# Performance work log

Hardware: AMD Instinct MI355X
Metric: run time of the kernel (lower is better)

The kernel has to match this reference:

```python
import jax, jax.numpy as jnp
import numpy as np
from jax import lax


def setup_inputs() -> dict:
    key = jax.random.key(0)
    ks = jax.random.split(key, 12)
    B, T_dec, T_enc, E, H, V = 32, 64, 128, 256, 512, 32000
    s = 0.05
    emb_W = jax.random.normal(ks[0], (V, E), jnp.float32) * s
    emb_W = emb_W.at[0].set(0.0)  # padding_idx=0
    return {
        "dec_X": jax.random.randint(ks[1], (B, T_dec), 0, V, dtype=jnp.int64),
        "enc_output": jax.random.normal(ks[2], (B, T_enc, H), jnp.float32),
        "h0": jax.random.normal(ks[3], (1, B, H), jnp.float32),
        "c0": jax.random.normal(ks[4], (1, B, H), jnp.float32),
        "emb_W": emb_W,
        "W_ih": jax.random.normal(ks[5], (4 * H, E), jnp.float32) * s,
        "W_hh": jax.random.normal(ks[6], (4 * H, H), jnp.float32) * s,
        "b_ih": jax.random.normal(ks[7], (4 * H,), jnp.float32) * s,
        "b_hh": jax.random.normal(ks[8], (4 * H,), jnp.float32) * s,
        "attn_W": jax.random.normal(ks[9], (H, 2 * H), jnp.float32) * s,
        "attn_b": jax.random.normal(ks[10], (H,), jnp.float32) * s,
        "fc_W": jax.random.normal(ks[11], (V, H), jnp.float32) * s,
        "fc_b": jnp.zeros((V,), jnp.float32),
    }


def reference(dec_X, enc_output, h0, c0, emb_W, W_ih, W_hh, b_ih, b_hh,
              attn_W, attn_b, fc_W, fc_b):
    # Embedding lookup for all decoder steps at once; padding_idx=0 -> zero vector.
    emb = emb_W[dec_X] * (dec_X != 0)[..., None].astype(emb_W.dtype)  # [B, T_dec, E]
    h, c = h0[0], c0[0]  # [B, H] (num_layers == 1)
    bias = b_ih + b_hh

    def step(carry, x_t):  # x_t: [B, E]
        h, c = carry
        g = x_t @ W_ih.T + h @ W_hh.T + bias          # [B, 4H]
        i, f, gg, o = jnp.split(g, 4, axis=-1)        # torch gate order i,f,g,o
        c = jax.nn.sigmoid(f) * c + jax.nn.sigmoid(i) * jnp.tanh(gg)
        h = jax.nn.sigmoid(o) * jnp.tanh(c)           # dec_rnn_out
        # dot-product attention over encoder timesteps (softmax over dim 1)
        scores = jnp.einsum('bth,bh->bt', enc_output, h)   # [B, T_enc]
        a = jax.nn.softmax(scores, axis=1)
        c_t = jnp.einsum('bt,bth->bh', a, enc_output)       # [B, H]
        cat = jnp.concatenate([h, c_t], axis=-1)            # [B, 2H]
        out = jnp.tanh(cat @ attn_W.T + attn_b)             # [B, H]
        logits = out @ fc_W.T + fc_b                        # [B, V]
        return (h, c), logits

    (h, c), logits = lax.scan(step, (h, c), jnp.swapaxes(emb, 0, 1))
    output = jnp.swapaxes(logits, 0, 1)  # [B, T_dec, V]
    return output, (h[None], c[None])
```

## Files before the change

kernel.cpp:

```cpp
#include <hip/hip_runtime.h>
#include <cstdint>
#include <cstddef>

typedef unsigned short u16;
typedef short s8v __attribute__((ext_vector_type(8)));
typedef float f4v __attribute__((ext_vector_type(4)));

static __device__ __forceinline__ u16 f2bf(float x) {
  union { float f; uint32_t u; } v; v.f = x;
  uint32_t r = v.u + 0x7fffu + ((v.u >> 16) & 1u);
  return (u16)(r >> 16);
}
static __device__ __forceinline__ uint2 f2bf4(float4 v) {
  uint2 r;
  r.x = (uint32_t)f2bf(v.x) | ((uint32_t)f2bf(v.y) << 16);
  r.y = (uint32_t)f2bf(v.z) | ((uint32_t)f2bf(v.w) << 16);
  return r;
}
static __device__ __forceinline__ float sigm(float x) { return 1.0f / (1.0f + __expf(-x)); }

typedef __attribute__((address_space(3))) uint32_t lds_u32;
typedef const __attribute__((address_space(1))) uint32_t glb_u32;
static __device__ __forceinline__ void gload16(const void* g, void* l) {
  __builtin_amdgcn_global_load_lds((glb_u32*)g, (lds_u32*)l, 16, 0, 0);
}

__global__ void kPrep(const float* __restrict__ fcW, const float* __restrict__ attnW,
                      const float* __restrict__ Wih, const float* __restrict__ bih,
                      const float* __restrict__ bhh, const float* __restrict__ embW,
                      const int* __restrict__ decX,
                      u16* __restrict__ fcWb, u16* __restrict__ attnWb, u16* __restrict__ Wihb,
                      u16* __restrict__ embg, float* __restrict__ biassum,
                      int* __restrict__ syncp) {
  const long NF4 = 4096000L, NA4 = 131072L, NW4 = 131072L, NE4 = 131072L, NB = 2048L, NS = 1024L;
  const long total = NF4 + NA4 + NW4 + NE4 + NB + NS;
  for (long i = (long)blockIdx.x * blockDim.x + threadIdx.x; i < total;
       i += (long)gridDim.x * blockDim.x) {
    if (i < NF4) {
      ((uint2*)fcWb)[i] = f2bf4(((const float4*)fcW)[i]);
    } else if (i < NF4 + NA4) {
      long k = i - NF4;
      ((uint2*)attnWb)[k] = f2bf4(((const float4*)attnW)[k]);
    } else if (i < NF4 + NA4 + NW4) {
      long k = i - NF4 - NA4;
      ((uint2*)Wihb)[k] = f2bf4(((const float4*)Wih)[k]);
    } else if (i < NF4 + NA4 + NW4 + NE4) {
      long k = i - NF4 - NA4 - NW4;
      int row = (int)(k >> 6), e4 = (int)(k & 63);
      int t = row >> 5, b = row & 31;
      int x = decX[b * 64 + t];
      float4 v = *(const float4*)&embW[(long)x * 256 + e4 * 4];
      ((uint2*)embg)[k] = f2bf4(v);
    } else if (i < NF4 + NA4 + NW4 + NE4 + NB) {
      long k = i - NF4 - NA4 - NW4 - NE4;
      biassum[k] = bih[k] + bhh[k];
    } else {
      long k = i - NF4 - NA4 - NW4 - NE4 - NB;
      syncp[k] = 0;
    }
  }
}

template <int ACT, int OUTBF, int SWZ>
__global__ __launch_bounds__(256) void kGemm(const u16* __restrict__ A, const u16* __restrict__ Bm,
                                             const float* __restrict__ bias,
                                             float* __restrict__ Cf, u16* __restrict__ Cb,
                                             int N, int K) {
  __shared__ u16 lA[8 * 64 * 8];
  __shared__ u16 lB[8 * 64 * 8];
  const int tid = threadIdx.x;
  int bxx = blockIdx.x, byy = blockIdx.y;
  if (SWZ) {
    int id = byy * gridDim.x + bxx;
    int cpx = (gridDim.x * gridDim.y) >> 3;
    int l = (id & 7) * cpx + (id >> 3);
    bxx = l % gridDim.x; byy = l / gridDim.x;
  }
  const int m0 = bxx * 128, n0 = byy * 128;
  const int lane = tid & 63, wid = tid >> 6;
  const int wm = wid >> 1, wn = wid & 1;
  f4v acc[4][4] = {};
  const int nkt = K >> 5;
  for (int kt = 0; kt < nkt; ++kt) {
    const int k0 = kt << 5;
#pragma unroll
    for (int i = 0; i < 2; ++i) {
      const int d = i * 4 + wid;
      const int m = (d << 4) | (lane & 15);
      const int q = lane >> 4;
      gload16(A + (size_t)(m0 + m) * K + k0 + q * 8, &lA[(i * 256 + wid * 64) * 8]);
      gload16(Bm + (size_t)(n0 + m) * K + k0 + q * 8, &lB[(i * 256 + wid * 64) * 8]);
    }
    __syncthreads();
    s8v af[4], bfr[4];
#pragma unroll
    for (int i = 0; i < 4; ++i) af[i] = *(const s8v*)&lA[((wm * 4 + i) * 64 + lane) * 8];
#pragma unroll
    for (int j = 0; j < 4; ++j) bfr[j] = *(const s8v*)&lB[((wn * 4 + j) * 64 + lane) * 8];
#pragma unroll
    for (int i = 0; i < 4; ++i)
#pragma unroll
      for (int j = 0; j < 4; ++j)
        acc[i][j] = __builtin_amdgcn_mfma_f32_16x16x32_bf16(af[i], bfr[j], acc[i][j], 0, 0, 0);
    __syncthreads();
  }
  const int rq = lane >> 4, cl = lane & 15;
#pragma unroll
  for (int j = 0; j < 4; ++j) {
    int col = n0 + wn * 64 + j * 16 + cl;
    float bv = bias[col];
#pragma unroll
    for (int i = 0; i < 4; ++i) {
      int rowb = m0 + wm * 64 + i * 16 + rq * 4;
      f4v v = acc[i][j];
#pragma unroll
      for (int r = 0; r < 4; ++r) {
        float x = v[r] + bv;
        if (ACT) x = tanhf(x);
        size_t off = (size_t)(rowb + r) * N + col;
        if (OUTBF) Cb[off] = f2bf(x); else Cf[off] = x;
      }
    }
  }
}

__global__ __launch_bounds__(256, 1) void kLSTM4(const float* __restrict__ Gpre,
                                                 const float* __restrict__ Whh,
                                                 const float* __restrict__ h0,
                                                 const float* __restrict__ c0,
                                                 float* __restrict__ Hall,
                                                 float* __restrict__ hx,
                                                 float* __restrict__ cx,
                                                 int* __restrict__ syncp) {
  __shared__ float4 hl4[5160];
  __shared__ int srank;
  const int tid = threadIdx.x;

  int xcc;
  asm volatile("s_getreg_b32 %0, hwreg(HW_REG_XCC_ID)" : "=s"(xcc));
  xcc &= 7;
  if (tid == 0) srank = atomicAdd(&syncp[xcc * 64], 1);
  __syncthreads();
  const int rank = srank & 31;
  const int j0 = rank * 16;
  const int b0 = xcc * 4;
  int* cnt = &syncp[(8 + xcc) * 64];

  const int jj = tid >> 4;
  const int ks = tid & 15;
  const int g_o = ks >> 2, bb_o = ks & 3;
  const int b_o = b0 + bb_o;
  const int j_o = j0 + jj;
  const bool cellLane = (g_o == 0);

  const float4* W4 = (const float4*)Whh;
  float4 Wr[4][8];
#pragma unroll
  for (int g = 0; g < 4; ++g) {
    const int row = g * 512 + j0 + jj;
#pragma unroll
    for (int i = 0; i < 8; ++i) Wr[g][i] = W4[(size_t)row * 128 + ks + 16 * i];
  }

  float creg = cellLane ? c0[b_o * 512 + j_o] : 0.f;
  const float4* hsrc = (const float4*)h0;
  float gpv = Gpre[(size_t)b_o * 2048 + (size_t)g_o * 512 + j_o];

  for (int t = 0; t < 64; ++t) {
#pragma unroll
    for (int it = 0; it < 2; ++it) {
      int idx = it * 256 + tid;
      int hb = idx >> 7, k4 = idx & 127;
      hl4[idx] = hsrc[(b0 + hb) * 128 + k4];
    }
    __syncthreads();

    float gnext = 0.f;
    if (t < 63)
      gnext = Gpre[((size_t)(t + 1) * 32 + b_o) * 2048 + (size_t)g_o * 512 + j_o];

    float acc[16];
#pragma unroll
    for (int p = 0; p < 16; ++p) acc[p] = 0.f;
#pragma unroll
    for (int i = 0; i < 8; ++i) {
      float4 h4[4];
#pragma unroll
      for (int bb = 0; bb < 4; ++bb) h4[bb] = hl4[bb * 128 + ks + 16 * i];
#pragma unroll
      for (int g = 0; g < 4; ++g) {
        float4 w = Wr[g][i];
#pragma unroll
        for (int bb = 0; bb < 4; ++bb)
          acc[g * 4 + bb] += w.x * h4[bb].x + w.y * h4[bb].y + w.z * h4[bb].z + w.w * h4[bb].w;
      }
    }

#define FOLD_STAGE(OFF, NN)                                        \
    {                                                              \
      const bool hi = (ks & OFF) != 0;                             \
      _Pragma("unroll")                                            \
      for (int q = 0; q < NN; ++q) {                               \
        float keepv = hi ? acc[q + NN] : acc[q];                   \
        float sendv = hi ? acc[q] : acc[q + NN];                   \
        acc[q] = keepv + __shfl_xor(sendv, OFF, 64);               \
      }                                                            \
    }
    FOLD_STAGE(8, 8)
    FOLD_STAGE(4, 4)
    FOLD_STAGE(2, 2)
    FOLD_STAGE(1, 1)
#undef FOLD_STAGE

    float pre = acc[0] + gpv;
    float v = (g_o == 2) ? tanhf(pre) : sigm(pre);
    float fv = __shfl_xor(v, 4, 64);
    float gv = __shfl_xor(v, 8, 64);
    float ov = __shfl_xor(v, 12, 64);
    float* hdst = Hall + (size_t)t * 16384;
    if (cellLane) {
      creg = fv * creg + v * gv;
      float hv = ov * tanhf(creg);
      hdst[b_o * 512 + j_o] = hv;
      if (t == 63) { hx[b_o * 512 + j_o] = hv; cx[b_o * 512 + j_o] = creg; }
    }
    __syncthreads();

    if (t < 63) {
      if (tid == 0) {
        unsigned one = 1u;
        asm volatile("global_atomic_add %0, %1, off"
                     :: "v"(cnt), "v"(one) : "memory");
        const int target = 32 * (t + 1);
        unsigned zero = 0u, old;
        for (;;) {
          asm volatile("global_atomic_add %0, %1, %2, off sc0\n\t"
                       "s_waitcnt vmcnt(0)"
                       : "=v"(old) : "v"(cnt), "v"(zero) : "memory");
          if ((int)old >= target) break;
          __builtin_amdgcn_s_sleep(1);
        }
      }
      __syncthreads();
    }
    gpv = gnext;
    hsrc = (const float4*)hdst;
  }
}

__global__ __launch_bounds__(256) void kAttn(const float* __restrict__ Hall, const float* __restrict__ enc,
                                             u16* __restrict__ CAT) {
  const int bx = blockIdx.x;
  const int b = bx >> 3, tg = bx & 7;
  const int tid = threadIdx.x;
  __shared__ float sh[8][516];
  __shared__ float sa[8][132];
  __shared__ float red[8][32];
  for (int tt = 0; tt < 8; ++tt) {
    int t = tg * 8 + tt;
    const float* hr = Hall + ((size_t)t * 32 + b) * 512;
    u16* cr = CAT + ((size_t)(b * 64 + t)) * 1024;
    for (int k = tid; k < 512; k += 256) { float v = hr[k]; sh[tt][k] = v; cr[k] = f2bf(v); }
  }
  __syncthreads();
  {
    const int tl = tid & 7, eb = tid >> 3;
#pragma unroll
    for (int u = 0; u < 4; ++u) {
      int e = eb + u * 32;
      const float* er = enc + ((size_t)b * 128 + e) * 512;
      float a = 0.f;
      for (int k = 0; k < 512; k += 4) {
        float4 ev = *(const float4*)&er[k];
        float4 hv = *(const float4*)&sh[tl][k];
        a += ev.x * hv.x + ev.y * hv.y + ev.z * hv.z + ev.w * hv.w;
      }
      sa[tl][e] = a;
    }
  }
  __syncthreads();
  {
    const int g = tid >> 5, l = tid & 31;
    float mx = -1e30f;
#pragma unroll
    for (int u = 0; u < 4; ++u) mx = fmaxf(mx, sa[g][l + u * 32]);
    red[g][l] = mx;
    __syncthreads();
    if (l == 0) {
      float m2 = -1e30f;
      for (int i = 0; i < 32; ++i) m2 = fmaxf(m2, red[g][i]);
      sa[g][128] = m2;
    }
    __syncthreads();
    float m2 = sa[g][128];
    float s = 0.f;
#pragma unroll
    for (int u = 0; u < 4; ++u) { int e = l + u * 32; float p = __expf(sa[g][e] - m2); sa[g][e] = p; s += p; }
    red[g][l] = s;
    __syncthreads();
    if (l == 0) {
      float s2 = 0.f;
      for (int i = 0; i < 32; ++i) s2 += red[g][i];
      sa[g][129] = 1.0f / s2;
    }
    __syncthreads();
    float inv = sa[g][129];
#pragma unroll
    for (int u = 0; u < 4; ++u) sa[g][l + u * 32] *= inv;
  }
  __syncthreads();
  {
    float a0[8], a1[8];
#pragma unroll
    for (int tt = 0; tt < 8; ++tt) { a0[tt] = 0.f; a1[tt] = 0.f; }
    const float* eb2 = enc + (size_t)b * 128 * 512 + tid * 2;
    for (int e = 0; e < 128; ++e) {
      float2 v = *(const float2*)&eb2[(size_t)e * 512];
#pragma unroll
      for (int tt = 0; tt < 8; ++tt) { float a = sa[tt][e]; a0[tt] += a * v.x; a1[tt] += a * v.y; }
    }
#pragma unroll
    for (int tt = 0; tt < 8; ++tt) {
      int t = tg * 8 + tt;
      u16* cr = CAT + ((size_t)(b * 64 + t)) * 1024 + 512;
      cr[tid * 2] = f2bf(a0[tt]); cr[tid * 2 + 1] = f2bf(a1[tt]);
    }
  }
}

extern "C" void kernel_launch(void* const* d_in, const int* in_sizes, int n_in,
                              void* d_out, int out_size, void* d_ws, size_t ws_size,
                              hipStream_t stream) {
  const int*   decX  = (const int*)d_in[0];
  const float* enc   = (const float*)d_in[1];
  const float* h0    = (const float*)d_in[2];
  const float* c0    = (const float*)d_in[3];
  const float* embW  = (const float*)d_in[4];
  const float* Wih   = (const float*)d_in[5];
  const float* Whh   = (const float*)d_in[6];
  const float* bih   = (const float*)d_in[7];
  const float* bhh   = (const float*)d_in[8];
  const float* attnW = (const float*)d_in[9];
  const float* attnb = (const float*)d_in[10];
  const float* fcW   = (const float*)d_in[11];
  const float* fcb   = (const float*)d_in[12];
  float* out = (float*)d_out;

  char* ws = (char*)d_ws;
  u16*   fcWb    = (u16*)(ws);
  u16*   attnWb  = (u16*)(ws + 32768000);
  u16*   Wihb    = (u16*)(ws + 33816576);
  u16*   embg    = (u16*)(ws + 34865152);
  float* biassum = (float*)(ws + 35913728);
  float* Gpre    = (float*)(ws + 35921920);
  float* Hall    = (float*)(ws + 52699136);
  u16*   CAT     = (u16*)(ws + 56893440);
  u16*   OUTb    = (u16*)(ws + 61087744);
  int*   syncp   = (int*)(ws + 63184896);

  hipLaunchKernelGGL(kPrep, dim3(4096), dim3(256), 0, stream,
                     fcW, attnW, Wih, bih, bhh, embW, decX, fcWb, attnWb, Wihb, embg, biassum,
                     syncp);
  hipLaunchKernelGGL((kGemm<0, 0, 0>), dim3(16, 16), dim3(256), 0, stream,
                     embg, Wihb, biassum, Gpre, (u16*)nullptr, 2048, 256);
  {
    float* hx = out + 65536000L;
    float* cx = out + 65536000L + 16384L;
    const float* gpreA = Gpre; const float* whhA = Whh;
    const float* h0A = h0;     const float* c0A = c0;
    float* hallA = Hall;       int* syncA = syncp;
    void* args[] = {(void*)&gpreA, (void*)&whhA, (void*)&h0A, (void*)&c0A,
                    (void*)&hallA, (void*)&hx, (void*)&cx, (void*)&syncA};
    hipLaunchCooperativeKernel((void*)kLSTM4, dim3(256), dim3(256), args, 0, stream);
  }
  hipLaunchKernelGGL(kAttn, dim3(256), dim3(256), 0, stream, Hall, enc, CAT);
  hipLaunchKernelGGL((kGemm<1, 1, 0>), dim3(16, 4), dim3(256), 0, stream,
                     CAT, attnWb, attnb, (float*)nullptr, OUTb, 512, 1024);
  hipLaunchKernelGGL((kGemm<0, 0, 1>), dim3(16, 250), dim3(256), 0, stream,
                     OUTb, fcWb, fcb, out, (u16*)nullptr, 32000, 512);
}
```

Measured before the change: 854.9 us.

## Use 256-row tiles for vocab GEMM and 512-thread LSTM blocks, drop swizzle

Adds kGemmL, a vocab-projection GEMM with 256x128 tiles in which each wave covers a full 64x128 strip. This doubles reuse of each loaded fcW tile and halves the grid. The LSTM recurrence kernel now runs 512 threads per block, which halves the per-thread W_hh register slice and the dot-product length, at the cost of one extra cross-half shuffle reduction. The XCC-aware block swizzle for the large GEMM is removed, which may reduce L2 locality.

New measurement: 894.7 us. 4.7% more time.

```diff
diff --git a/kernel.cpp b/kernel.cpp
--- a/kernel.cpp
+++ b/kernel.cpp
@@ -61,7 +61,7 @@
   }
 }
 
-template <int ACT, int OUTBF, int SWZ>
+template <int ACT, int OUTBF>
 __global__ __launch_bounds__(256) void kGemm(const u16* __restrict__ A, const u16* __restrict__ Bm,
                                              const float* __restrict__ bias,
                                              float* __restrict__ Cf, u16* __restrict__ Cb,
@@ -69,14 +69,7 @@
   __shared__ u16 lA[8 * 64 * 8];
   __shared__ u16 lB[8 * 64 * 8];
   const int tid = threadIdx.x;
-  int bxx = blockIdx.x, byy = blockIdx.y;
-  if (SWZ) {
-    int id = byy * gridDim.x + bxx;
-    int cpx = (gridDim.x * gridDim.y) >> 3;
-    int l = (id & 7) * cpx + (id >> 3);
-    bxx = l % gridDim.x; byy = l / gridDim.x;
-  }
-  const int m0 = bxx * 128, n0 = byy * 128;
+  const int m0 = blockIdx.x * 128, n0 = blockIdx.y * 128;
   const int lane = tid & 63, wid = tid >> 6;
   const int wm = wid >> 1, wn = wid & 1;
   f4v acc[4][4] = {};
@@ -124,7 +117,59 @@
   }
 }
 
-__global__ __launch_bounds__(256, 1) void kLSTM4(const float* __restrict__ Gpre,
+__global__ __launch_bounds__(256) void kGemmL(const u16* __restrict__ A, const u16* __restrict__ Bm,
+                                              const float* __restrict__ bias,
+                                              float* __restrict__ Cf, int N, int K) {
+  __shared__ u16 lA[16 * 64 * 8];
+  __shared__ u16 lB[8 * 64 * 8];
+  const int tid = threadIdx.x;
+  const int m0 = blockIdx.x * 256, n0 = blockIdx.y * 128;
+  const int lane = tid & 63, wid = tid >> 6;
+  f4v acc[4][8] = {};
+  const int nkt = K >> 5;
+  for (int kt = 0; kt < nkt; ++kt) {
+    const int k0 = kt << 5;
+    const int mq = (lane & 15), q = lane >> 4;
+#pragma unroll
+    for (int i = 0; i < 4; ++i) {
+      const int m = ((i * 4 + wid) << 4) | mq;
+      gload16(A + (size_t)(m0 + m) * K + k0 + q * 8, &lA[(i * 256 + wid * 64) * 8]);
+    }
+#pragma unroll
+    for (int i = 0; i < 2; ++i) {
+      const int m = ((i * 4 + wid) << 4) | mq;
+      gload16(Bm + (size_t)(n0 + m) * K + k0 + q * 8, &lB[(i * 256 + wid * 64) * 8]);
+    }
+    __syncthreads();
+    s8v af[4], bfr[8];
+#pragma unroll
+    for (int i = 0; i < 4; ++i) af[i] = *(const s8v*)&lA[((wid * 4 + i) * 64 + lane) * 8];
+#pragma unroll
+    for (int j = 0; j < 8; ++j) bfr[j] = *(const s8v*)&lB[(j * 64 + lane) * 8];
+#pragma unroll
+    for (int i = 0; i < 4; ++i)
+#pragma unroll
+      for (int j = 0; j < 8; ++j)
+        acc[i][j] = __builtin_amdgcn_mfma_f32_16x16x32_bf16(af[i], bfr[j], acc[i][j], 0, 0, 0);
+    __syncthreads();
+  }
+  const int rq = lane >> 4, cl = lane & 15;
+#pragma unroll
+  for (int j = 0; j < 8; ++j) {
+    int col = n0 + j * 16 + cl;
+    float bv = bias[col];
+#pragma unroll
+    for (int i = 0; i < 4; ++i) {
+      int rowb = m0 + wid * 64 + i * 16 + rq * 4;
+      f4v v = acc[i][j];
+#pragma unroll
+      for (int r = 0; r < 4; ++r)
+        Cf[(size_t)(rowb + r) * N + col] = v[r] + bv;
+    }
+  }
+}
+
+__global__ __launch_bounds__(512, 1) void kLSTM5(const float* __restrict__ Gpre,
                                                  const float* __restrict__ Whh,
                                                  const float* __restrict__ h0,
                                                  const float* __restrict__ c0,
@@ -146,47 +191,43 @@
   const int b0 = xcc * 4;
   int* cnt = &syncp[(8 + xcc) * 64];
 
-  const int jj = tid >> 4;
-  const int ks = tid & 15;
-  const int g_o = ks >> 2, bb_o = ks & 3;
+  const int jj = tid >> 5;
+  const int ks = tid & 31;
+  const int g_o = (ks >> 2) & 3, bb_o = ks & 3;
   const int b_o = b0 + bb_o;
   const int j_o = j0 + jj;
-  const bool cellLane = (g_o == 0);
+  const bool outLane = (ks < 16);
+  const bool cellLane = (ks < 4);
 
   const float4* W4 = (const float4*)Whh;
-  float4 Wr[4][8];
+  float4 Wr[4][4];
 #pragma unroll
   for (int g = 0; g < 4; ++g) {
     const int row = g * 512 + j0 + jj;
 #pragma unroll
-    for (int i = 0; i < 8; ++i) Wr[g][i] = W4[(size_t)row * 128 + ks + 16 * i];
+    for (int i = 0; i < 4; ++i) Wr[g][i] = W4[(size_t)row * 128 + ks + 32 * i];
   }
 
   float creg = cellLane ? c0[b_o * 512 + j_o] : 0.f;
   const float4* hsrc = (const float4*)h0;
-  float gpv = Gpre[(size_t)b_o * 2048 + (size_t)g_o * 512 + j_o];
+  float gpv = outLane ? Gpre[(size_t)b_o * 2048 + (size_t)g_o * 512 + j_o] : 0.f;
 
   for (int t = 0; t < 64; ++t) {
-#pragma unroll
-    for (int it = 0; it < 2; ++it) {
-      int idx = it * 256 + tid;
-      int hb = idx >> 7, k4 = idx & 127;
-      hl4[idx] = hsrc[(b0 + hb) * 128 + k4];
-    }
+    hl4[tid] = hsrc[(b0 + (tid >> 7)) * 128 + (tid & 127)];
     __syncthreads();
 
     float gnext = 0.f;
-    if (t < 63)
+    if (outLane && t < 63)
       gnext = Gpre[((size_t)(t + 1) * 32 + b_o) * 2048 + (size_t)g_o * 512 + j_o];
 
     float acc[16];
 #pragma unroll
     for (int p = 0; p < 16; ++p) acc[p] = 0.f;
 #pragma unroll
-    for (int i = 0; i < 8; ++i) {
+    for (int i = 0; i < 4; ++i) {
       float4 h4[4];
 #pragma unroll
-      for (int bb = 0; bb < 4; ++bb) h4[bb] = hl4[bb * 128 + ks + 16 * i];
+      for (int bb = 0; bb < 4; ++bb) h4[bb] = hl4[bb * 128 + ks + 32 * i];
 #pragma unroll
       for (int g = 0; g < 4; ++g) {
         float4 w = Wr[g][i];
@@ -196,6 +237,8 @@
       }
     }
 
+#pragma unroll
+    for (int q = 0; q < 16; ++q) acc[q] += __shfl_xor(acc[q], 16, 64);
 #define FOLD_STAGE(OFF, NN)                                        \
     {                                                              \
       const bool hi = (ks & OFF) != 0;                             \
@@ -361,7 +404,7 @@
   hipLaunchKernelGGL(kPrep, dim3(4096), dim3(256), 0, stream,
                      fcW, attnW, Wih, bih, bhh, embW, decX, fcWb, attnWb, Wihb, embg, biassum,
                      syncp);
-  hipLaunchKernelGGL((kGemm<0, 0, 0>), dim3(16, 16), dim3(256), 0, stream,
+  hipLaunchKernelGGL((kGemm<0, 0>), dim3(16, 16), dim3(256), 0, stream,
                      embg, Wihb, biassum, Gpre, (u16*)nullptr, 2048, 256);
   {
     float* hx = out + 65536000L;
@@ -371,11 +414,11 @@
     float* hallA = Hall;       int* syncA = syncp;
     void* args[] = {(void*)&gpreA, (void*)&whhA, (void*)&h0A, (void*)&c0A,
                     (void*)&hallA, (void*)&hx, (void*)&cx, (void*)&syncA};
-    hipLaunchCooperativeKernel((void*)kLSTM4, dim3(256), dim3(256), args, 0, stream);
+    hipLaunchCooperativeKernel((void*)kLSTM5, dim3(256), dim3(512), args, 0, stream);
   }
   hipLaunchKernelGGL(kAttn, dim3(256), dim3(256), 0, stream, Hall, enc, CAT);
-  hipLaunchKernelGGL((kGemm<1, 1, 0>), dim3(16, 4), dim3(256), 0, stream,
+  hipLaunchKernelGGL((kGemm<1, 1>), dim3(16, 4), dim3(256), 0, stream,
                      CAT, attnWb, attnb, (float*)nullptr, OUTb, 512, 1024);
-  hipLaunchKernelGGL((kGemm<0, 0, 1>), dim3(16, 250), dim3(256), 0, stream,
-                     OUTb, fcWb, fcb, out, (u16*)nullptr, 32000, 512);
-}
+  hipLaunchKernelGGL(kGemmL, dim3(8, 250), dim3(256), 0, stream,
+                     OUTb, fcWb, fcb, out, 32000, 512);
+}
```
